# Performance work log

Hardware: AMD Instinct MI355X
Metric: run time of the kernel (lower is better)

## Reference

```python
import jax, jax.numpy as jnp
import numpy as np

N = 8192; E = 262144
CS = 384; CZ = 128; CH = 16; H = 12; PQK = 4; PV = 8
INF = 1e5; EPS = 1e-8
S_QK = float(1.0 / np.sqrt(3.0 * CH))        # sqrt(1/(3*c_hidden))
S_B = float(1.0 / np.sqrt(3.0))              # sqrt(1/3)
S_PT = float(1.0 / np.sqrt(3.0 * (PQK * 9.0 / 2.0)))


def setup_inputs() -> dict:
    key = jax.random.key(0)
    ks = jax.random.split(key, 16)
    def w(k, shape, fan_in):
        return jax.random.normal(k, shape, jnp.float32) * (1.0 / float(np.sqrt(fan_in)))
    d = {}
    d["s"] = jax.random.normal(ks[0], (N, CS), jnp.float32)
    d["z"] = jax.random.normal(ks[1], (E, CZ), jnp.float32)
    d["edge_index"] = jax.random.randint(ks[2], (2, E), 0, N, jnp.int32)
    d["rot"] = jax.random.normal(ks[3], (N, 3, 3), jnp.float32)
    d["trans"] = jax.random.normal(ks[4], (N, 3), jnp.float32)
    d["mask"] = jnp.ones((N,), jnp.float32)
    d["q_w"] = w(ks[5], (CS, H * CH), CS);              d["q_b"] = jnp.zeros((H * CH,), jnp.float32)
    d["kv_w"] = w(ks[6], (CS, 2 * H * CH), CS);         d["kv_b"] = jnp.zeros((2 * H * CH,), jnp.float32)
    d["qp_w"] = w(ks[7], (CS, H * PQK * 3), CS);        d["qp_b"] = jnp.zeros((H * PQK * 3,), jnp.float32)
    d["kvp_w"] = w(ks[8], (CS, H * (PQK + PV) * 3), CS); d["kvp_b"] = jnp.zeros((H * (PQK + PV) * 3,), jnp.float32)
    d["b_w"] = w(ks[9], (CZ, H), CZ);                   d["b_b"] = jnp.zeros((H,), jnp.float32)
    d["dz_w"] = w(ks[10], (CZ, CZ // 4), CZ);           d["dz_b"] = jnp.zeros((CZ // 4,), jnp.float32)
    d["head_weights"] = jnp.full((H,), float(np.log(np.e - 1.0)), jnp.float32)
    cdim = H * (CZ // 4 + CH + PV * 4)
    d["out_w"] = w(ks[11], (cdim, CS), cdim);           d["out_b"] = jnp.zeros((CS,), jnp.float32)
    return d


def reference(s, z, edge_index, rot, trans, mask,
              q_w, q_b, kv_w, kv_b, qp_w, qp_b, kvp_w, kvp_b,
              b_w, b_b, dz_w, dz_b, head_weights, out_w, out_b):
    src = edge_index[1]
    dst = edge_index[0]

    def to_pts(y, P):
        # y: [N, H*P*3] -> split into (x,y,z) chunks -> [N, H*P, 3], then rigid-apply
        xyz = jnp.stack(jnp.split(y, 3, axis=-1), axis=-1)          # [N, H*P, 3]
        pts = jnp.einsum('nij,npj->npi', rot, xyz) + trans[:, None, :]
        return pts.reshape(N, H, P, 3)

    q = (s @ q_w + q_b).reshape(N, H, CH)
    kv = (s @ kv_w + kv_b).reshape(N, H, 2 * CH)
    k, v = kv[..., :CH], kv[..., CH:]

    q_pts = to_pts(s @ qp_w + qp_b, PQK)                            # [N,H,PQK,3]
    kv_pts = to_pts(s @ kvp_w + kvp_b, PQK + PV)                    # [N,H,PQK+PV,3]
    k_pts, v_pts = kv_pts[..., :PQK, :], kv_pts[..., PQK:, :]

    b = z @ b_w + b_b                                               # [E, H]

    # scalar attention logits
    a = jnp.einsum('ehc,ehc->eh', q[src], k[dst]) * S_QK + S_B * b  # [E, H]

    # point attention logits
    disp = q_pts[src] - k_pts[dst]                                  # [E,H,PQK,3]
    pt_att = jnp.sum(disp * disp, axis=-1)                          # [E,H,PQK]
    hw = jax.nn.softplus(head_weights) * S_PT                       # [H]
    pt_att = -0.5 * jnp.sum(pt_att * hw[None, :, None], axis=-1)    # [E,H]

    edge_mask = INF * (mask[dst] * mask[src] - 1.0)                 # [E]
    a = a + pt_att + edge_mask[:, None]

    # scatter softmax over src segments (pyg-style)
    amax = jax.ops.segment_max(a, src, num_segments=N)
    amax = jnp.where(jnp.isfinite(amax), amax, 0.0)
    ex = jnp.exp(a - amax[src])
    denom = jax.ops.segment_sum(ex, src, num_segments=N)
    a = ex / (denom[src] + 1e-16)                                   # [E,H]

    # weighted scatter-reduce aggregations
    o = jax.ops.segment_sum(a[..., None] * v[dst], src, num_segments=N).reshape(N, H * CH)
    o_pt = jax.ops.segment_sum(a[..., None, None] * v_pts[dst], src, num_segments=N)  # [N,H,PV,3]
    # invert_apply: R^T (p - t)
    o_pt = jnp.einsum('nji,nhpj->nhpi', rot, o_pt - trans[:, None, None, :])
    o_pt_norm = jnp.sqrt(jnp.sum(o_pt * o_pt, axis=-1) + EPS).reshape(N, H * PV)
    o_pt_flat = o_pt.reshape(N, H * PV, 3)

    pair_z = z @ dz_w + dz_b                                        # [E, CZ//4]
    o_pair = jax.ops.segment_sum(a[..., None] * pair_z[:, None, :], src, num_segments=N).reshape(N, H * (CZ // 4))

    feats = jnp.concatenate(
        [o, o_pt_flat[..., 0], o_pt_flat[..., 1], o_pt_flat[..., 2], o_pt_norm, o_pair], axis=-1)
    return feats @ out_w + out_b
```

## Files before the change

### kernel.cpp

```cpp
#include <hip/hip_runtime.h>
#include <math.h>

#define NN 8192
#define EE 262144
#define CSD 384
#define CZD 128
#define HH 12
#define MAXDEG 96
#define ABLD 13

#define S_QK 0.14433756729740643f
#define S_B  0.5773502691896258f
#define S_PT 0.1360827634879543f

typedef __bf16 bf16;
typedef __attribute__((ext_vector_type(8))) __bf16 bf16x8;
typedef __attribute__((ext_vector_type(4))) __bf16 bf16x4;
typedef __attribute__((ext_vector_type(4))) float floatx4;

#define OFF_LIN    0
#define OFF_QPACK  (OFF_LIN + NN*1152)
#define OFF_KPACKH (OFF_QPACK + NN*336)
#define OFF_VPACKH (OFF_KPACKH + NN*192)
#define OFF_BLOG   (OFF_VPACKH + NN*240)
#define OFF_PAIRH  (OFF_BLOG + EE*12)
#define OFF_SBF    (OFF_PAIRH + EE*16)
#define OFF_WCAT   (OFF_SBF + NN*192)
#define OFF_OWT    (OFF_WCAT + 221184)
#define OFF_FEATB  (OFF_OWT + 184320)
#define OFF_BZW    (OFF_FEATB + NN*480)
#define OFF_BZB    (OFF_BZW + 3072)
#define OFF_BIASC  (OFF_BZB + 48)
#define OFF_INTS   (OFF_BIASC + 1152)

__global__ void count_kernel(const int* __restrict__ ei, int* __restrict__ counts) {
    int e = blockIdx.x * 256 + threadIdx.x;
    if (e < EE) atomicAdd(&counts[ei[EE + e]], 1);
}

__global__ __launch_bounds__(1024) void scan_kernel(const int* __restrict__ counts,
                                                    int* __restrict__ offs,
                                                    int* __restrict__ cursor) {
    __shared__ int part[1024];
    int t = threadIdx.x;
    int local[8];
    int s = 0;
    #pragma unroll
    for (int j = 0; j < 8; ++j) { local[j] = counts[t * 8 + j]; s += local[j]; }
    part[t] = s;
    __syncthreads();
    for (int off = 1; off < 1024; off <<= 1) {
        int vv = 0;
        if (t >= off) vv = part[t - off];
        __syncthreads();
        if (t >= off) part[t] += vv;
        __syncthreads();
    }
    int run = (t == 0) ? 0 : part[t - 1];
    #pragma unroll
    for (int j = 0; j < 8; ++j) {
        offs[t * 8 + j] = run;
        cursor[t * 8 + j] = run;
        run += local[j];
    }
    if (t == 1023) offs[NN] = run;
}

__global__ void fill_kernel(const int* __restrict__ ei, int* __restrict__ cursor,
                            int* __restrict__ elist) {
    int e = blockIdx.x * 256 + threadIdx.x;
    if (e < EE) {
        int s = ei[EE + e];
        int pos = atomicAdd(&cursor[s], 1);
        elist[pos] = e;
    }
}

__global__ __launch_bounds__(1024) void sort_kernel(const int* __restrict__ offs,
                                                    int* __restrict__ order) {
    __shared__ int hist[256];
    __shared__ int base[256];
    int t = threadIdx.x;
    if (t < 256) hist[t] = 0;
    __syncthreads();
    for (int n = t; n < NN; n += 1024) {
        int d = offs[n + 1] - offs[n];
        if (d > 255) d = 255;
        atomicAdd(&hist[d], 1);
    }
    __syncthreads();
    if (t == 0) {
        int run = 0;
        for (int d = 255; d >= 0; --d) { base[d] = run; run += hist[d]; }
    }
    __syncthreads();
    for (int n = t; n < NN; n += 1024) {
        int d = offs[n + 1] - offs[n];
        if (d > 255) d = 255;
        int pos = atomicAdd(&base[d], 1);
        order[pos] = n;
    }
}

__global__ void cvt_s_kernel(const float* __restrict__ s, bf16* __restrict__ sbf) {
    int i = blockIdx.x * 256 + threadIdx.x;
    float4 v = *(const float4*)(s + (long)i * 4);
    bf16x4 o = {(__bf16)v.x, (__bf16)v.y, (__bf16)v.z, (__bf16)v.w};
    *(bf16x4*)(sbf + (long)i * 4) = o;
}

__global__ void build_wcat(const float* __restrict__ q_w, const float* __restrict__ kv_w,
                           const float* __restrict__ qp_w, const float* __restrict__ kvp_w,
                           const float* __restrict__ q_b, const float* __restrict__ kv_b,
                           const float* __restrict__ qp_b, const float* __restrict__ kvp_b,
                           bf16* __restrict__ wt, float* __restrict__ bias_cat) {
    int id = blockIdx.x * 256 + threadIdx.x;
    if (id >= 1152 * 384) return;
    int n = id / 384, k = id - n * 384;
    float v;
    if (n < 192)      v = q_w[k * 192 + n];
    else if (n < 576) v = kv_w[k * 384 + (n - 192)];
    else if (n < 720) v = qp_w[k * 144 + (n - 576)];
    else              v = kvp_w[k * 432 + (n - 720)];
    wt[id] = (__bf16)v;
    if (k == 0) {
        float b;
        if (n < 192)      b = q_b[n];
        else if (n < 576) b = kv_b[n - 192];
        else if (n < 720) b = qp_b[n - 576];
        else              b = kvp_b[n - 720];
        bias_cat[n] = b;
    }
}

__global__ void build_owt(const float* __restrict__ out_w, bf16* __restrict__ wt) {
    int id = blockIdx.x * 256 + threadIdx.x;
    if (id >= 384 * 960) return;
    int n = id / 960, k = id - n * 960;
    wt[id] = (__bf16)out_w[k * 384 + n];
}

__global__ void build_bzw(const float* __restrict__ b_w, const float* __restrict__ b_b,
                          const float* __restrict__ dz_w, const float* __restrict__ dz_b,
                          bf16* __restrict__ wt, float* __restrict__ bias) {
    int id = blockIdx.x * 256 + threadIdx.x;
    if (id < 48 * 128) {
        int c = id / 128, k = id - c * 128;
        float v = 0.f;
        if (c < 12)      v = b_w[k * 12 + c];
        else if (c < 44) v = dz_w[k * 32 + (c - 12)];
        wt[id] = (__bf16)v;
    }
    if (id < 44) bias[id] = (id < 12) ? b_b[id] : dz_b[id - 12];
}

#define LDKP 40
__global__ __launch_bounds__(256) void gemm_mfma_bt(const bf16* __restrict__ A,
                                                    const bf16* __restrict__ BT,
                                                    const float* __restrict__ bias,
                                                    float* __restrict__ C,
                                                    int M, int K, int N) {
    __shared__ __align__(16) bf16 As[128][LDKP];
    __shared__ __align__(16) bf16 Bs[128][LDKP];
    const int tid = threadIdx.x;
    const int bm = blockIdx.y * 128;
    const int bn = blockIdx.x * 128;
    const int wave = tid >> 6, lane = tid & 63;
    const int wr = (wave >> 1) * 64;
    const int wc = (wave & 1) * 64;
    const int lm = lane & 15;
    const int kg = lane >> 4;

    floatx4 acc[4][4];
    #pragma unroll
    for (int i = 0; i < 4; ++i)
        #pragma unroll
        for (int j = 0; j < 4; ++j) acc[i][j] = (floatx4){0.f, 0.f, 0.f, 0.f};

    const int srow = tid >> 2;
    const int skoff = (tid & 3) * 8;

    for (int k0 = 0; k0 < K; k0 += 32) {
        __syncthreads();
        *(float4*)(&As[srow][skoff])      = *(const float4*)(A + (long)(bm + srow) * K + k0 + skoff);
        *(float4*)(&As[srow + 64][skoff]) = *(const float4*)(A + (long)(bm + srow + 64) * K + k0 + skoff);
        *(float4*)(&Bs[srow][skoff])      = *(const float4*)(BT + (long)(bn + srow) * K + k0 + skoff);
        *(float4*)(&Bs[srow + 64][skoff]) = *(const float4*)(BT + (long)(bn + srow + 64) * K + k0 + skoff);
        __syncthreads();
        bf16x8 af[4], bfr[4];
        #pragma unroll
        for (int i = 0; i < 4; ++i) af[i] = *(const bf16x8*)(&As[wr + i * 16 + lm][kg * 8]);
        #pragma unroll
        for (int j = 0; j < 4; ++j) bfr[j] = *(const bf16x8*)(&Bs[wc + j * 16 + lm][kg * 8]);
        #pragma unroll
        for (int i = 0; i < 4; ++i)
            #pragma unroll
            for (int j = 0; j < 4; ++j)
                acc[i][j] = __builtin_amdgcn_mfma_f32_16x16x32_bf16(af[i], bfr[j], acc[i][j], 0, 0, 0);
    }

    const int crow0 = bm + wr + kg * 4;
    const int ccol0 = bn + wc + lm;
    #pragma unroll
    for (int i = 0; i < 4; ++i) {
        #pragma unroll
        for (int j = 0; j < 4; ++j) {
            int col = ccol0 + j * 16;
            float b = bias[col];
            #pragma unroll
            for (int r = 0; r < 4; ++r)
                C[(long)(crow0 + i * 16 + r) * N + col] = acc[i][j][r] + b;
        }
    }
}

#define BZLD 136
__global__ __launch_bounds__(256) void gemm_bz(const float* __restrict__ z,
                                               const bf16* __restrict__ BT,
                                               const float* __restrict__ bias,
                                               float* __restrict__ blog,
                                               bf16* __restrict__ pairh) {
    __shared__ __align__(16) bf16 As[128][BZLD];
    __shared__ __align__(16) bf16 Bs[48][BZLD];
    const int tid = threadIdx.x;
    const int bm = blockIdx.x * 128;
    {
        int row = tid >> 1, half = tid & 1;
        const float* zr = z + (long)(bm + row) * 128 + half * 64;
        #pragma unroll
        for (int j = 0; j < 8; ++j) {
            float4 a0 = *(const float4*)(zr + j * 8);
            float4 a1 = *(const float4*)(zr + j * 8 + 4);
            bf16x8 o = {(__bf16)a0.x, (__bf16)a0.y, (__bf16)a0.z, (__bf16)a0.w,
                        (__bf16)a1.x, (__bf16)a1.y, (__bf16)a1.z, (__bf16)a1.w};
            *(bf16x8*)(&As[row][half * 64 + j * 8]) = o;
        }
    }
    for (int idx = tid; idx < 48 * 16; idx += 256) {
        int r = idx >> 4, seg = idx & 15;
        *(bf16x8*)(&Bs[r][seg * 8]) = *(const bf16x8*)(BT + r * 128 + seg * 8);
    }
    __syncthreads();
    const int wave = tid >> 6, lane = tid & 63;
    const int lm = lane & 15, kg = lane >> 4;
    const int rowbase = wave * 32;
    floatx4 acc[2][3];
    #pragma unroll
    for (int i = 0; i < 2; ++i)
        #pragma unroll
        for (int j = 0; j < 3; ++j) acc[i][j] = (floatx4){0.f, 0.f, 0.f, 0.f};
    #pragma unroll
    for (int ks = 0; ks < 4; ++ks) {
        bf16x8 af[2], bfr[3];
        #pragma unroll
        for (int i = 0; i < 2; ++i) af[i] = *(const bf16x8*)(&As[rowbase + i * 16 + lm][ks * 32 + kg * 8]);
        #pragma unroll
        for (int j = 0; j < 3; ++j) bfr[j] = *(const bf16x8*)(&Bs[j * 16 + lm][ks * 32 + kg * 8]);
        #pragma unroll
        for (int i = 0; i < 2; ++i)
            #pragma unroll
            for (int j = 0; j < 3; ++j)
                acc[i][j] = __builtin_amdgcn_mfma_f32_16x16x32_bf16(af[i], bfr[j], acc[i][j], 0, 0, 0);
    }
    #pragma unroll
    for (int i = 0; i < 2; ++i) {
        int r0 = bm + rowbase + i * 16 + kg * 4;
        #pragma unroll
        for (int j = 0; j < 3; ++j) {
            int col = j * 16 + lm;
            if (col < 12) {
                float b = bias[col];
                #pragma unroll
                for (int r = 0; r < 4; ++r)
                    blog[(long)(r0 + r) * 12 + col] = acc[i][j][r] + b;
            } else if (col < 44) {
                float b = bias[col];
                #pragma unroll
                for (int r = 0; r < 4; ++r)
                    pairh[(long)(r0 + r) * 32 + (col - 12)] = (__bf16)(acc[i][j][r] + b);
            }
        }
    }
}

__global__ void pack_kernel(const float* __restrict__ lin,
                            const float* __restrict__ rot, const float* __restrict__ trans,
                            float* __restrict__ qpack, bf16* __restrict__ kpackh,
                            bf16* __restrict__ vpackh) {
    int n = blockIdx.x;
    int t = threadIdx.x;
    const float* row = lin + (long)n * 1152;
    const float* R = rot + n * 9;
    float tx = trans[n * 3 + 0], ty = trans[n * 3 + 1], tz = trans[n * 3 + 2];
    {
        int h = t >> 4, c = t & 15;
        qpack[(long)n * 336 + h * 28 + c] = row[h * 16 + c];
        kpackh[(long)n * 384 + h * 32 + c] = (__bf16)row[192 + h * 32 + c];
        vpackh[(long)n * 480 + h * 40 + c] = (__bf16)row[192 + h * 32 + 16 + c];
    }
    if (t < 48 && (t & 3) == 0) {
        int h = t >> 2;
        #pragma unroll
        for (int j = 0; j < 4; ++j) kpackh[(long)n * 384 + h * 32 + 28 + j] = (__bf16)0.f;
    }
    float x, y, z;
    if (t < 48) {
        x = row[576 + t]; y = row[624 + t]; z = row[672 + t];
    } else {
        int u = t - 48;
        x = row[720 + u]; y = row[864 + u]; z = row[1008 + u];
    }
    float ox = R[0] * x + R[1] * y + R[2] * z + tx;
    float oy = R[3] * x + R[4] * y + R[5] * z + ty;
    float oz = R[6] * x + R[7] * y + R[8] * z + tz;
    if (t < 48) {
        int h = t >> 2, p = t & 3;
        long b = (long)n * 336 + h * 28 + 16 + p * 3;
        qpack[b] = ox; qpack[b + 1] = oy; qpack[b + 2] = oz;
    } else {
        int u = t - 48;
        int h = u / 12, j = u - h * 12;
        if (j < 4) {
            long b = (long)n * 384 + h * 32 + 16 + j * 3;
            kpackh[b] = (__bf16)ox; kpackh[b + 1] = (__bf16)oy; kpackh[b + 2] = (__bf16)oz;
        } else {
            long b = (long)n * 480 + h * 40 + 16 + (j - 4) * 3;
            vpackh[b] = (__bf16)ox; vpackh[b + 1] = (__bf16)oy; vpackh[b + 2] = (__bf16)oz;
        }
    }
}

__global__ __launch_bounds__(256) void agg_fused(const int* __restrict__ offs,
                                                 const int* __restrict__ elist,
                                                 const int* __restrict__ ei,
                                                 const int* __restrict__ order,
                                                 const float* __restrict__ qpack,
                                                 const bf16* __restrict__ kpackh,
                                                 const bf16* __restrict__ vpackh,
                                                 const float* __restrict__ blog,
                                                 const bf16* __restrict__ pairh,
                                                 const float* __restrict__ mask,
                                                 const float* __restrict__ head_w,
                                                 const float* __restrict__ rot,
                                                 const float* __restrict__ trans,
                                                 bf16* __restrict__ feats) {
    const int wave = threadIdx.x >> 6;
    const int lane = threadIdx.x & 63;
    const int n = order[blockIdx.x * 4 + wave];

    __shared__ float abuf_all[4][MAXDEG * ABLD];
    __shared__ __align__(16) float q_all[4][352];
    __shared__ int   emeta_all[4][MAXDEG];
    __shared__ int   dmeta_all[4][MAXDEG];
    __shared__ float mmeta_all[4][MAXDEG];
    float* abuf  = abuf_all[wave];
    float* q_s   = q_all[wave];
    int*   emeta = emeta_all[wave];
    int*   dmeta = dmeta_all[wave];
    float* mmeta = mmeta_all[wave];

    const int beg = offs[n];
    int deg = offs[n + 1] - beg;
    if (deg > MAXDEG) deg = MAXDEG;

    for (int idx = lane; idx < 84; idx += 64)
        *(float4*)(&q_s[idx * 4]) = *(const float4*)(qpack + (long)n * 336 + idx * 4);
    if (lane < 12) q_s[336 + lane] = log1pf(expf(head_w[lane])) * S_PT;
    const float msrc = mask[n];

    if (lane < deg) {
        int e = elist[beg + lane];
        int d = ei[e];
        emeta[lane] = e; dmeta[lane] = d; mmeta[lane] = mask[d];
    }
    if (64 + lane < deg) {
        int e = elist[beg + 64 + lane];
        int d = ei[e];
        emeta[64 + lane] = e; dmeta[64 + lane] = d; mmeta[64 + lane] = mask[d];
    }
    __syncthreads();

    for (int idx = lane; idx < deg * 12; idx += 64) {
        int c = idx / 12, h = idx - c * 12;
        int e = emeta[c];
        int d = dmeta[c];
        float md = mmeta[c];
        const bf16* khp = kpackh + (long)d * 384 + h * 32;
        bf16x8 k0 = *(const bf16x8*)khp;
        bf16x8 k1 = *(const bf16x8*)(khp + 8);
        bf16x8 p0 = *(const bf16x8*)(khp + 16);
        bf16x8 p1 = *(const bf16x8*)(khp + 24);
        const float* qh = &q_s[h * 28];
        float qk = 0.f, pt = 0.f;
        #pragma unroll
        for (int i = 0; i < 8; ++i) qk += qh[i] * (float)k0[i];
        #pragma unroll
        for (int i = 0; i < 8; ++i) qk += qh[8 + i] * (float)k1[i];
        #pragma unroll
        for (int i = 0; i < 8; ++i) { float dd = qh[16 + i] - (float)p0[i]; pt += dd * dd; }
        #pragma unroll
        for (int i = 0; i < 4; ++i) { float dd = qh[24 + i] - (float)p1[i]; pt += dd * dd; }
        float b = blog[(long)e * 12 + h];
        abuf[c * ABLD + h] = qk * S_QK + S_B * b - 0.5f * q_s[336 + h] * pt
                           + 100000.0f * (msrc * md - 1.0f);
    }
    __syncthreads();

    {
        float lg0[12], lg1[12];
        const bool a0 = lane < deg, a1 = 64 + lane < deg;
        #pragma unroll
        for (int h = 0; h < 12; ++h) {
            lg0[h] = a0 ? abuf[lane * ABLD + h] : -1e30f;
            lg1[h] = a1 ? abuf[(64 + lane) * ABLD + h] : -1e30f;
        }
        #pragma unroll
        for (int h = 0; h < 12; ++h) {
            float mx = fmaxf(lg0[h], lg1[h]);
            #pragma unroll
            for (int off = 32; off > 0; off >>= 1) mx = fmaxf(mx, __shfl_xor(mx, off));
            if (!isfinite(mx)) mx = 0.f;
            float w0 = a0 ? __expf(lg0[h] - mx) : 0.f;
            float w1 = a1 ? __expf(lg1[h] - mx) : 0.f;
            float sm = w0 + w1;
            #pragma unroll
            for (int off = 32; off > 0; off >>= 1) sm += __shfl_xor(sm, off);
            float rl = 1.f / (sm + 1e-16f);
            if (a0) abuf[lane * ABLD + h] = w0 * rl;
            if (a1) abuf[(64 + lane) * ABLD + h] = w1 * rl;
        }
    }
    __syncthreads();

    int hh[2], off8[2];
    bool pr[2], act[2];
    #pragma unroll
    for (int r = 0; r < 2; ++r) {
        int slot = r * 64 + lane;
        if (slot < 60) {
            hh[r] = slot / 5;
            off8[r] = hh[r] * 40 + (slot - hh[r] * 5) * 8;
            pr[r] = false; act[r] = true;
        } else if (slot < 108) {
            int u2 = slot - 60;
            hh[r] = u2 >> 2;
            off8[r] = (u2 & 3) * 8;
            pr[r] = true; act[r] = true;
        } else {
            hh[r] = 0; off8[r] = 0; pr[r] = false; act[r] = false;
        }
    }
    float acc[2][8];
    #pragma unroll
    for (int r = 0; r < 2; ++r)
        #pragma unroll
        for (int i = 0; i < 8; ++i) acc[r][i] = 0.f;

    #pragma unroll 2
    for (int c = 0; c < deg; ++c) {
        int eC = emeta[c];
        int dC = dmeta[c];
        const bf16* vpb = vpackh + (long)dC * 480;
        const bf16* ppb = pairh + (long)eC * 32;
        #pragma unroll
        for (int r = 0; r < 2; ++r) {
            if (act[r]) {
                float w = abuf[c * ABLD + hh[r]];
                bf16x8 v = *(const bf16x8*)((pr[r] ? ppb : vpb) + off8[r]);
                #pragma unroll
                for (int i = 0; i < 8; ++i) acc[r][i] += w * (float)v[i];
            }
        }
    }

    float* opt_s = q_s;
    #pragma unroll
    for (int r = 0; r < 2; ++r) {
        if (!act[r]) continue;
        int slot = r * 64 + lane;
        if (!pr[r]) {
            int h = hh[r], u = slot - h * 5;
            if (u < 2) {
                bf16* fp = feats + (long)n * 960 + h * 16 + u * 8;
                bf16x4 o1 = {(__bf16)acc[r][0], (__bf16)acc[r][1], (__bf16)acc[r][2], (__bf16)acc[r][3]};
                bf16x4 o2 = {(__bf16)acc[r][4], (__bf16)acc[r][5], (__bf16)acc[r][6], (__bf16)acc[r][7]};
                *(bf16x4*)fp = o1;
                *(bf16x4*)(fp + 4) = o2;
            } else {
                float* op = &opt_s[h * 24 + (u - 2) * 8];
                *(floatx4*)op = (floatx4){acc[r][0], acc[r][1], acc[r][2], acc[r][3]};
                *(floatx4*)(op + 4) = (floatx4){acc[r][4], acc[r][5], acc[r][6], acc[r][7]};
            }
        } else {
            int u2 = slot - 60, h = u2 >> 2, seg = u2 & 3;
            bf16* fp = feats + (long)n * 960 + 576 + h * 32 + seg * 8;
            bf16x4 o1 = {(__bf16)acc[r][0], (__bf16)acc[r][1], (__bf16)acc[r][2], (__bf16)acc[r][3]};
            bf16x4 o2 = {(__bf16)acc[r][4], (__bf16)acc[r][5], (__bf16)acc[r][6], (__bf16)acc[r][7]};
            *(bf16x4*)fp = o1;
            *(bf16x4*)(fp + 4) = o2;
        }
    }
    __syncthreads();

    const float* R = rot + n * 9;
    float tx = trans[n * 3 + 0], ty = trans[n * 3 + 1], tz = trans[n * 3 + 2];
    for (int idx = lane; idx < 96; idx += 64) {
        int h = idx >> 3, p = idx & 7;
        float x = opt_s[h * 24 + p * 3 + 0] - tx;
        float y = opt_s[h * 24 + p * 3 + 1] - ty;
        float zc = opt_s[h * 24 + p * 3 + 2] - tz;
        float ox = R[0] * x + R[3] * y + R[6] * zc;
        float oy = R[1] * x + R[4] * y + R[7] * zc;
        float oz = R[2] * x + R[5] * y + R[8] * zc;
        float nrm = sqrtf(ox * ox + oy * oy + oz * oz + 1e-8f);
        feats[(long)n * 960 + 192 + idx] = (__bf16)ox;
        feats[(long)n * 960 + 288 + idx] = (__bf16)oy;
        feats[(long)n * 960 + 384 + idx] = (__bf16)oz;
        feats[(long)n * 960 + 480 + idx] = (__bf16)nrm;
    }
}

extern "C" void kernel_launch(void* const* d_in, const int* in_sizes, int n_in,
                              void* d_out, int out_size, void* d_ws, size_t ws_size,
                              hipStream_t stream) {
    const float* s      = (const float*)d_in[0];
    const float* z      = (const float*)d_in[1];
    const int*   ei     = (const int*)d_in[2];
    const float* rot    = (const float*)d_in[3];
    const float* trans  = (const float*)d_in[4];
    const float* mask   = (const float*)d_in[5];
    const float* q_w    = (const float*)d_in[6];
    const float* q_b    = (const float*)d_in[7];
    const float* kv_w   = (const float*)d_in[8];
    const float* kv_b   = (const float*)d_in[9];
    const float* qp_w   = (const float*)d_in[10];
    const float* qp_b   = (const float*)d_in[11];
    const float* kvp_w  = (const float*)d_in[12];
    const float* kvp_b  = (const float*)d_in[13];
    const float* b_w    = (const float*)d_in[14];
    const float* b_b    = (const float*)d_in[15];
    const float* dz_w   = (const float*)d_in[16];
    const float* dz_b   = (const float*)d_in[17];
    const float* head_w = (const float*)d_in[18];
    const float* out_w  = (const float*)d_in[19];
    const float* out_b  = (const float*)d_in[20];

    float* ws      = (float*)d_ws;
    float* lin     = ws + OFF_LIN;
    float* qpack   = ws + OFF_QPACK;
    bf16*  kpackh  = (bf16*)(ws + OFF_KPACKH);
    bf16*  vpackh  = (bf16*)(ws + OFF_VPACKH);
    float* blog    = ws + OFF_BLOG;
    bf16*  pairh   = (bf16*)(ws + OFF_PAIRH);
    bf16*  sbf     = (bf16*)(ws + OFF_SBF);
    bf16*  wcat    = (bf16*)(ws + OFF_WCAT);
    bf16*  owt     = (bf16*)(ws + OFF_OWT);
    bf16*  featb   = (bf16*)(ws + OFF_FEATB);
    bf16*  bzwbf   = (bf16*)(ws + OFF_BZW);
    float* bzb     = ws + OFF_BZB;
    float* biasc   = ws + OFF_BIASC;
    int* ints   = (int*)(ws + OFF_INTS);
    int* offs   = ints;
    int* cursor = ints + NN + 1;
    int* counts = ints + 2 * NN + 1;
    int* elist  = ints + 3 * NN + 1;
    int* order  = ints + 3 * NN + 1 + EE;

    hipMemsetAsync(counts, 0, NN * sizeof(int), stream);
    count_kernel<<<EE / 256, 256, 0, stream>>>(ei, counts);
    scan_kernel<<<1, 1024, 0, stream>>>(counts, offs, cursor);
    fill_kernel<<<EE / 256, 256, 0, stream>>>(ei, cursor, elist);
    sort_kernel<<<1, 1024, 0, stream>>>(offs, order);

    cvt_s_kernel<<<NN * CSD / 4 / 256, 256, 0, stream>>>(s, sbf);
    build_wcat<<<(1152 * 384 + 255) / 256, 256, 0, stream>>>(q_w, kv_w, qp_w, kvp_w,
                                                             q_b, kv_b, qp_b, kvp_b, wcat, biasc);
    build_owt<<<(384 * 960 + 255) / 256, 256, 0, stream>>>(out_w, owt);
    build_bzw<<<(48 * 128 + 255) / 256, 256, 0, stream>>>(b_w, b_b, dz_w, dz_b, bzwbf, bzb);

    gemm_mfma_bt<<<dim3(1152 / 128, NN / 128), 256, 0, stream>>>(sbf, wcat, biasc, lin, NN, CSD, 1152);

    pack_kernel<<<NN, 192, 0, stream>>>(lin, rot, trans, qpack, kpackh, vpackh);

    gemm_bz<<<EE / 128, 256, 0, stream>>>(z, bzwbf, bzb, blog, pairh);

    agg_fused<<<NN / 4, 256, 0, stream>>>(offs, elist, ei, order, qpack, kpackh, vpackh,
                                          blog, pairh, mask, head_w, rot, trans, featb);

    gemm_mfma_bt<<<dim3(384 / 128, NN / 128), 256, 0, stream>>>(featb, owt, out_b, (float*)d_out, NN, 960, 384);
}
```

Before: 462.2 us.

## Shrink aggregation LDS footprint and compute logits in registers with pair-split heads

The aggregation kernel packs edge id, destination and mask bit into one int, stores softmax weights as fp16 instead of fp32, and drops the separate logit buffer. Each lane pair now computes six heads of logits per edge and keeps them in registers for the softmax, which removes a round trip through shared memory and a sync. It also adds a launch-bounds occupancy hint. The bz GEMM now loads its A operand straight from global memory into registers, with no shared-memory staging. Risks are fp16 weight precision, the bit-packing limits on edge and node counts, and higher register pressure from the 3x6 logit array.

```diff
diff --git a/kernel.cpp b/kernel.cpp
--- a/kernel.cpp
+++ b/kernel.cpp
@@ -7,7 +7,7 @@
 #define CZD 128
 #define HH 12
 #define MAXDEG 96
-#define ABLD 13
+#define WLD 14
 
 #define S_QK 0.14433756729740643f
 #define S_B  0.5773502691896258f
@@ -220,22 +220,9 @@
                                                const float* __restrict__ bias,
                                                float* __restrict__ blog,
                                                bf16* __restrict__ pairh) {
-    __shared__ __align__(16) bf16 As[128][BZLD];
     __shared__ __align__(16) bf16 Bs[48][BZLD];
     const int tid = threadIdx.x;
     const int bm = blockIdx.x * 128;
-    {
-        int row = tid >> 1, half = tid & 1;
-        const float* zr = z + (long)(bm + row) * 128 + half * 64;
-        #pragma unroll
-        for (int j = 0; j < 8; ++j) {
-            float4 a0 = *(const float4*)(zr + j * 8);
-            float4 a1 = *(const float4*)(zr + j * 8 + 4);
-            bf16x8 o = {(__bf16)a0.x, (__bf16)a0.y, (__bf16)a0.z, (__bf16)a0.w,
-                        (__bf16)a1.x, (__bf16)a1.y, (__bf16)a1.z, (__bf16)a1.w};
-            *(bf16x8*)(&As[row][half * 64 + j * 8]) = o;
-        }
-    }
     for (int idx = tid; idx < 48 * 16; idx += 256) {
         int r = idx >> 4, seg = idx & 15;
         *(bf16x8*)(&Bs[r][seg * 8]) = *(const bf16x8*)(BT + r * 128 + seg * 8);
@@ -253,7 +240,13 @@
     for (int ks = 0; ks < 4; ++ks) {
         bf16x8 af[2], bfr[3];
         #pragma unroll
-        for (int i = 0; i < 2; ++i) af[i] = *(const bf16x8*)(&As[rowbase + i * 16 + lm][ks * 32 + kg * 8]);
+        for (int i = 0; i < 2; ++i) {
+            const float* zp = z + (long)(bm + rowbase + i * 16 + lm) * 128 + ks * 32 + kg * 8;
+            float4 a0 = *(const float4*)zp;
+            float4 a1 = *(const float4*)(zp + 4);
+            af[i] = (bf16x8){(__bf16)a0.x, (__bf16)a0.y, (__bf16)a0.z, (__bf16)a0.w,
+                             (__bf16)a1.x, (__bf16)a1.y, (__bf16)a1.z, (__bf16)a1.w};
+        }
         #pragma unroll
         for (int j = 0; j < 3; ++j) bfr[j] = *(const bf16x8*)(&Bs[j * 16 + lm][ks * 32 + kg * 8]);
         #pragma unroll
@@ -330,7 +323,7 @@
     }
 }
 
-__global__ __launch_bounds__(256) void agg_fused(const int* __restrict__ offs,
+__global__ __launch_bounds__(256, 6) void agg_fused(const int* __restrict__ offs,
                                                  const int* __restrict__ elist,
                                                  const int* __restrict__ ei,
                                                  const int* __restrict__ order,
@@ -348,16 +341,12 @@
     const int lane = threadIdx.x & 63;
     const int n = order[blockIdx.x * 4 + wave];
 
-    __shared__ float abuf_all[4][MAXDEG * ABLD];
     __shared__ __align__(16) float q_all[4][352];
-    __shared__ int   emeta_all[4][MAXDEG];
-    __shared__ int   dmeta_all[4][MAXDEG];
-    __shared__ float mmeta_all[4][MAXDEG];
-    float* abuf  = abuf_all[wave];
-    float* q_s   = q_all[wave];
-    int*   emeta = emeta_all[wave];
-    int*   dmeta = dmeta_all[wave];
-    float* mmeta = mmeta_all[wave];
+    __shared__ int smeta_all[4][MAXDEG];
+    __shared__ _Float16 wbuf_all[4][MAXDEG * WLD];
+    float*    q_s   = q_all[wave];
+    int*      smeta = smeta_all[wave];
+    _Float16* wbuf  = wbuf_all[wave];
 
     const int beg = offs[n];
     int deg = offs[n + 1] - beg;
@@ -371,64 +360,84 @@
     if (lane < deg) {
         int e = elist[beg + lane];
         int d = ei[e];
-        emeta[lane] = e; dmeta[lane] = d; mmeta[lane] = mask[d];
+        unsigned mb = (mask[d] != 0.f) ? 1u : 0u;
+        smeta[lane] = (int)(((unsigned)e << 14) | ((unsigned)d << 1) | mb);
     }
     if (64 + lane < deg) {
         int e = elist[beg + 64 + lane];
         int d = ei[e];
-        emeta[64 + lane] = e; dmeta[64 + lane] = d; mmeta[64 + lane] = mask[d];
-    }
-    __syncthreads();
-
-    for (int idx = lane; idx < deg * 12; idx += 64) {
-        int c = idx / 12, h = idx - c * 12;
-        int e = emeta[c];
-        int d = dmeta[c];
-        float md = mmeta[c];
-        const bf16* khp = kpackh + (long)d * 384 + h * 32;
-        bf16x8 k0 = *(const bf16x8*)khp;
-        bf16x8 k1 = *(const bf16x8*)(khp + 8);
-        bf16x8 p0 = *(const bf16x8*)(khp + 16);
-        bf16x8 p1 = *(const bf16x8*)(khp + 24);
-        const float* qh = &q_s[h * 28];
-        float qk = 0.f, pt = 0.f;
-        #pragma unroll
-        for (int i = 0; i < 8; ++i) qk += qh[i] * (float)k0[i];
-        #pragma unroll
-        for (int i = 0; i < 8; ++i) qk += qh[8 + i] * (float)k1[i];
-        #pragma unroll
-        for (int i = 0; i < 8; ++i) { float dd = qh[16 + i] - (float)p0[i]; pt += dd * dd; }
-        #pragma unroll
-        for (int i = 0; i < 4; ++i) { float dd = qh[24 + i] - (float)p1[i]; pt += dd * dd; }
-        float b = blog[(long)e * 12 + h];
-        abuf[c * ABLD + h] = qk * S_QK + S_B * b - 0.5f * q_s[336 + h] * pt
-                           + 100000.0f * (msrc * md - 1.0f);
-    }
-    __syncthreads();
-
-    {
-        float lg0[12], lg1[12];
-        const bool a0 = lane < deg, a1 = 64 + lane < deg;
-        #pragma unroll
-        for (int h = 0; h < 12; ++h) {
-            lg0[h] = a0 ? abuf[lane * ABLD + h] : -1e30f;
-            lg1[h] = a1 ? abuf[(64 + lane) * ABLD + h] : -1e30f;
-        }
-        #pragma unroll
-        for (int h = 0; h < 12; ++h) {
-            float mx = fmaxf(lg0[h], lg1[h]);
-            #pragma unroll
-            for (int off = 32; off > 0; off >>= 1) mx = fmaxf(mx, __shfl_xor(mx, off));
-            if (!isfinite(mx)) mx = 0.f;
-            float w0 = a0 ? __expf(lg0[h] - mx) : 0.f;
-            float w1 = a1 ? __expf(lg1[h] - mx) : 0.f;
-            float sm = w0 + w1;
-            #pragma unroll
-            for (int off = 32; off > 0; off >>= 1) sm += __shfl_xor(sm, off);
-            float rl = 1.f / (sm + 1e-16f);
-            if (a0) abuf[lane * ABLD + h] = w0 * rl;
-            if (a1) abuf[(64 + lane) * ABLD + h] = w1 * rl;
-        }
+        unsigned mb = (mask[d] != 0.f) ? 1u : 0u;
+        smeta[64 + lane] = (int)(((unsigned)e << 14) | ((unsigned)d << 1) | mb);
+    }
+    __syncthreads();
+
+    const int p = lane & 1;
+    const int hbase = 6 * p;
+    float lg[3][6];
+    #pragma unroll
+    for (int r = 0; r < 3; ++r)
+        #pragma unroll
+        for (int j = 0; j < 6; ++j) lg[r][j] = -1e30f;
+
+    #pragma unroll
+    for (int r = 0; r < 3; ++r) {
+        if (deg > r * 32) {
+            const int c = (r * 64 + lane) >> 1;
+            if (c < deg) {
+                const unsigned mm = (unsigned)smeta[c];
+                const int e = (int)(mm >> 14);
+                const int d = (int)((mm >> 1) & 8191u);
+                const float md = (float)(mm & 1u);
+                const float mterm = 100000.0f * (msrc * md - 1.0f);
+                const float* bl = blog + (long)e * 12 + hbase;
+                float blr[6];
+                *(float2*)(&blr[0]) = *(const float2*)(bl);
+                *(float2*)(&blr[2]) = *(const float2*)(bl + 2);
+                *(float2*)(&blr[4]) = *(const float2*)(bl + 4);
+                const bf16* kb = kpackh + (long)d * 384 + hbase * 32;
+                #pragma unroll
+                for (int j = 0; j < 6; ++j) {
+                    bf16x8 k0 = *(const bf16x8*)(kb + j * 32);
+                    bf16x8 k1 = *(const bf16x8*)(kb + j * 32 + 8);
+                    bf16x8 p0 = *(const bf16x8*)(kb + j * 32 + 16);
+                    bf16x8 p1 = *(const bf16x8*)(kb + j * 32 + 24);
+                    const float* qh = &q_s[(hbase + j) * 28];
+                    float qk = 0.f, pt = 0.f;
+                    #pragma unroll
+                    for (int i = 0; i < 8; ++i) qk += qh[i] * (float)k0[i];
+                    #pragma unroll
+                    for (int i = 0; i < 8; ++i) qk += qh[8 + i] * (float)k1[i];
+                    #pragma unroll
+                    for (int i = 0; i < 8; ++i) { float dd = qh[16 + i] - (float)p0[i]; pt += dd * dd; }
+                    #pragma unroll
+                    for (int i = 0; i < 4; ++i) { float dd = qh[24 + i] - (float)p1[i]; pt += dd * dd; }
+                    lg[r][j] = qk * S_QK + S_B * blr[j]
+                             - 0.5f * q_s[336 + hbase + j] * pt + mterm;
+                }
+            }
+        }
+    }
+
+    #pragma unroll
+    for (int j = 0; j < 6; ++j) {
+        float mx = fmaxf(fmaxf(lg[0][j], lg[1][j]), lg[2][j]);
+        #pragma unroll
+        for (int off = 2; off <= 32; off <<= 1) mx = fmaxf(mx, __shfl_xor(mx, off));
+        if (!isfinite(mx)) mx = 0.f;
+        float e0 = __expf(lg[0][j] - mx);
+        float e1 = __expf(lg[1][j] - mx);
+        float e2 = __expf(lg[2][j] - mx);
+        float sm = e0 + e1 + e2;
+        #pragma unroll
+        for (int off = 2; off <= 32; off <<= 1) sm += __shfl_xor(sm, off);
+        float rl = 1.f / (sm + 1e-16f);
+        const int h = hbase + j;
+        int c0 = lane >> 1;
+        if (c0 < deg) wbuf[c0 * WLD + h] = (_Float16)(e0 * rl);
+        int c1 = 32 + (lane >> 1);
+        if (c1 < deg) wbuf[c1 * WLD + h] = (_Float16)(e1 * rl);
+        int c2 = 64 + (lane >> 1);
+        if (c2 < deg) wbuf[c2 * WLD + h] = (_Float16)(e2 * rl);
     }
     __syncthreads();
 
@@ -458,14 +467,15 @@
 
     #pragma unroll 2
     for (int c = 0; c < deg; ++c) {
-        int eC = emeta[c];
-        int dC = dmeta[c];
+        const unsigned mm = (unsigned)smeta[c];
+        const int eC = (int)(mm >> 14);
+        const int dC = (int)((mm >> 1) & 8191u);
         const bf16* vpb = vpackh + (long)dC * 480;
         const bf16* ppb = pairh + (long)eC * 32;
         #pragma unroll
         for (int r = 0; r < 2; ++r) {
             if (act[r]) {
-                float w = abuf[c * ABLD + hh[r]];
+                float w = (float)wbuf[c * WLD + hh[r]];
                 bf16x8 v = *(const bf16x8*)((pr[r] ? ppb : vpb) + off8[r]);
                 #pragma unroll
                 for (int i = 0; i < 8; ++i) acc[r][i] += w * (float)v[i];
@@ -505,10 +515,10 @@
     const float* R = rot + n * 9;
     float tx = trans[n * 3 + 0], ty = trans[n * 3 + 1], tz = trans[n * 3 + 2];
     for (int idx = lane; idx < 96; idx += 64) {
-        int h = idx >> 3, p = idx & 7;
-        float x = opt_s[h * 24 + p * 3 + 0] - tx;
-        float y = opt_s[h * 24 + p * 3 + 1] - ty;
-        float zc = opt_s[h * 24 + p * 3 + 2] - tz;
+        int h = idx >> 3, pp = idx & 7;
+        float x = opt_s[h * 24 + pp * 3 + 0] - tx;
+        float y = opt_s[h * 24 + pp * 3 + 1] - ty;
+        float zc = opt_s[h * 24 + pp * 3 + 2] - tz;
         float ox = R[0] * x + R[3] * y + R[6] * zc;
         float oy = R[1] * x + R[4] * y + R[7] * zc;
         float oz = R[2] * x + R[5] * y + R[8] * zc;
```

After: 484.4 us. 1.05x slower.

## Pack edge metadata into one word, drop LDS staging in gemm_bz, raise occupancy

Applied to the files above, without the earlier changes.

In agg_fused, the edge id, destination node and mask bit are packed into one 32-bit word stored in a single shared array instead of three, which cuts LDS footprint and reads per edge. Launch bounds with a minimum of 6 blocks per SM are added to push the compiler toward higher occupancy. In gemm_bz, the A tile is read directly from global memory and converted to bf16 in registers, removing the As shared buffer and its sync staging. The bit packing assumes e < 2^18 and mask values that are exactly 0 or 1, and the launch-bounds hint may force register spills.

```diff
diff --git a/kernel.cpp b/kernel.cpp
--- a/kernel.cpp
+++ b/kernel.cpp
@@ -220,22 +220,9 @@
                                                const float* __restrict__ bias,
                                                float* __restrict__ blog,
                                                bf16* __restrict__ pairh) {
-    __shared__ __align__(16) bf16 As[128][BZLD];
     __shared__ __align__(16) bf16 Bs[48][BZLD];
     const int tid = threadIdx.x;
     const int bm = blockIdx.x * 128;
-    {
-        int row = tid >> 1, half = tid & 1;
-        const float* zr = z + (long)(bm + row) * 128 + half * 64;
-        #pragma unroll
-        for (int j = 0; j < 8; ++j) {
-            float4 a0 = *(const float4*)(zr + j * 8);
-            float4 a1 = *(const float4*)(zr + j * 8 + 4);
-            bf16x8 o = {(__bf16)a0.x, (__bf16)a0.y, (__bf16)a0.z, (__bf16)a0.w,
-                        (__bf16)a1.x, (__bf16)a1.y, (__bf16)a1.z, (__bf16)a1.w};
-            *(bf16x8*)(&As[row][half * 64 + j * 8]) = o;
-        }
-    }
     for (int idx = tid; idx < 48 * 16; idx += 256) {
         int r = idx >> 4, seg = idx & 15;
         *(bf16x8*)(&Bs[r][seg * 8]) = *(const bf16x8*)(BT + r * 128 + seg * 8);
@@ -253,7 +240,13 @@
     for (int ks = 0; ks < 4; ++ks) {
         bf16x8 af[2], bfr[3];
         #pragma unroll
-        for (int i = 0; i < 2; ++i) af[i] = *(const bf16x8*)(&As[rowbase + i * 16 + lm][ks * 32 + kg * 8]);
+        for (int i = 0; i < 2; ++i) {
+            const float* zp = z + (long)(bm + rowbase + i * 16 + lm) * 128 + ks * 32 + kg * 8;
+            float4 a0 = *(const float4*)zp;
+            float4 a1 = *(const float4*)(zp + 4);
+            af[i] = (bf16x8){(__bf16)a0.x, (__bf16)a0.y, (__bf16)a0.z, (__bf16)a0.w,
+                             (__bf16)a1.x, (__bf16)a1.y, (__bf16)a1.z, (__bf16)a1.w};
+        }
         #pragma unroll
         for (int j = 0; j < 3; ++j) bfr[j] = *(const bf16x8*)(&Bs[j * 16 + lm][ks * 32 + kg * 8]);
         #pragma unroll
@@ -330,7 +323,7 @@
     }
 }
 
-__global__ __launch_bounds__(256) void agg_fused(const int* __restrict__ offs,
+__global__ __launch_bounds__(256, 6) void agg_fused(const int* __restrict__ offs,
                                                  const int* __restrict__ elist,
                                                  const int* __restrict__ ei,
                                                  const int* __restrict__ order,
@@ -350,14 +343,10 @@
 
     __shared__ float abuf_all[4][MAXDEG * ABLD];
     __shared__ __align__(16) float q_all[4][352];
-    __shared__ int   emeta_all[4][MAXDEG];
-    __shared__ int   dmeta_all[4][MAXDEG];
-    __shared__ float mmeta_all[4][MAXDEG];
+    __shared__ int smeta_all[4][MAXDEG];
     float* abuf  = abuf_all[wave];
     float* q_s   = q_all[wave];
-    int*   emeta = emeta_all[wave];
-    int*   dmeta = dmeta_all[wave];
-    float* mmeta = mmeta_all[wave];
+    int*   smeta = smeta_all[wave];
 
     const int beg = offs[n];
     int deg = offs[n + 1] - beg;
@@ -371,20 +360,23 @@
     if (lane < deg) {
         int e = elist[beg + lane];
         int d = ei[e];
-        emeta[lane] = e; dmeta[lane] = d; mmeta[lane] = mask[d];
+        unsigned mb = (mask[d] != 0.f) ? 1u : 0u;
+        smeta[lane] = (int)(((unsigned)e << 14) | ((unsigned)d << 1) | mb);
     }
     if (64 + lane < deg) {
         int e = elist[beg + 64 + lane];
         int d = ei[e];
-        emeta[64 + lane] = e; dmeta[64 + lane] = d; mmeta[64 + lane] = mask[d];
+        unsigned mb = (mask[d] != 0.f) ? 1u : 0u;
+        smeta[64 + lane] = (int)(((unsigned)e << 14) | ((unsigned)d << 1) | mb);
     }
     __syncthreads();
 
     for (int idx = lane; idx < deg * 12; idx += 64) {
         int c = idx / 12, h = idx - c * 12;
-        int e = emeta[c];
-        int d = dmeta[c];
-        float md = mmeta[c];
+        const unsigned mm = (unsigned)smeta[c];
+        const int e = (int)(mm >> 14);
+        const int d = (int)((mm >> 1) & 8191u);
+        const float md = (float)(mm & 1u);
         const bf16* khp = kpackh + (long)d * 384 + h * 32;
         bf16x8 k0 = *(const bf16x8*)khp;
         bf16x8 k1 = *(const bf16x8*)(khp + 8);
@@ -458,8 +450,9 @@
 
     #pragma unroll 2
     for (int c = 0; c < deg; ++c) {
-        int eC = emeta[c];
-        int dC = dmeta[c];
+        const unsigned mm = (unsigned)smeta[c];
+        const int eC = (int)(mm >> 14);
+        const int dC = (int)((mm >> 1) & 8191u);
         const bf16* vpb = vpackh + (long)dC * 480;
         const bf16* ppb = pairh + (long)eC * 32;
         #pragma unroll
```

Result: no change. 470.3 us (+1.7%).
